# Kernel optimization log

Hardware: AMD Instinct MI355X
Metric: run time of the kernel (lower is better)

## Reference

```python
import jax, jax.numpy as jnp
import numpy as np

B, T, D = 1, 2048, 4096
N, K, H = 32, 8, 128
SLOTS = 32768
THETA = 500000.0
NEG_INF = -1e30


def apply_rope(x, positions, theta=THETA):
    # x: [B, heads, T, H]; positions: [T] int32. Llama half-split rotary.
    h = x.shape[-1]
    inv_freq = 1.0 / (theta ** (jnp.arange(0, h, 2, dtype=jnp.float32) / h))  # [H/2]
    ang = positions.astype(jnp.float32)[:, None] * inv_freq[None, :]          # [T, H/2]
    cos, sin = jnp.cos(ang), jnp.sin(ang)
    x1, x2 = x[..., : h // 2], x[..., h // 2 :]
    return jnp.concatenate([x1 * cos - x2 * sin, x2 * cos + x1 * sin], axis=-1).astype(x.dtype)


def setup_inputs() -> dict:
    key = jax.random.key(0)
    ks = jax.random.split(key, 5)
    x = jax.random.normal(ks[0], (B, T, D), jnp.float32)
    wq = jax.random.normal(ks[1], (N, D, H), jnp.float32) * (D ** -0.5)
    wk = jax.random.normal(ks[2], (K, D, H), jnp.float32) * (D ** -0.5)
    wv = jax.random.normal(ks[3], (K, D, H), jnp.float32) * (D ** -0.5)
    wo = jax.random.normal(ks[4], (N, H, D), jnp.float32) * ((N * H) ** -0.5)
    k_cache = jnp.zeros((SLOTS, K, H), jnp.float32)
    v_cache = jnp.zeros((SLOTS, K, H), jnp.float32)
    positions = jnp.arange(T, dtype=jnp.int32)
    write_indices = jnp.arange(T, dtype=jnp.int32)  # paged-cache slot per token, in [0, SLOTS)
    return dict(x=x, wq=wq, wk=wk, wv=wv, wo=wo, k_cache=k_cache, v_cache=v_cache,
                positions=positions, write_indices=write_indices)


def reference(x, wq, wk, wv, wo, k_cache, v_cache, positions, write_indices):
    # QKV projections (per-head einsum, as in the module)
    q = jnp.einsum('btd,ndh->bnth', x, wq)            # [B,N,T,H]
    k = jnp.einsum('btd,kdh->bkth', x, wk)            # [B,K,T,H]
    v = jnp.einsum('btd,kdh->bkth', x, wv)            # [B,K,T,H]
    # RoPE on q and k, then q scaling by head_dim**-0.5 (applied to q as in source)
    q = apply_rope(q, positions) * (H ** -0.5)
    k = apply_rope(k, positions)
    # KV-cache scatter write (B=1): cache layout [slot, kv_head, head_dim]
    k_cache = k_cache.at[write_indices].set(jnp.transpose(k[0], (1, 0, 2)))
    v_cache = v_cache.at[write_indices].set(jnp.transpose(v[0], (1, 0, 2)))
    # Prefill causal GQA attention over the current sequence
    g = N // K
    qg = q.reshape(B, K, g, T, H)
    scores = jnp.einsum('bkgth,bksh->bkgts', qg, k)   # [B,K,G,T,T]
    mask = positions[:, None] >= positions[None, :]   # causal
    scores = jnp.where(mask, scores, NEG_INF)
    p = jax.nn.softmax(scores, axis=-1)
    attn = jnp.einsum('bkgts,bksh->bkgth', p, v).reshape(B, N, T, H)
    o = jnp.einsum('bnth,nhd->btd', attn, wo)         # [B,T,D]
    return k_cache, v_cache, o
```

## Files before the change

### kernel.cpp

```cpp
#include <hip/hip_runtime.h>
#include <stdint.h>

#define T_SEQ   2048
#define D_MODEL 4096
#define NQ      32
#define NKV     8
#define HD      128
#define NSLOTS  32768
#define L2THETA_64 0.29580575976911624f
#define QSCALE_LOG2E 0.12751743126f

typedef __bf16 bf16;
typedef bf16  bf16x8 __attribute__((ext_vector_type(8)));
typedef float f32x4  __attribute__((ext_vector_type(4)));

#define AS1 __attribute__((address_space(1)))
#define AS3 __attribute__((address_space(3)))

__device__ __forceinline__ void async_ld16(const bf16* g, bf16* l) {
  __builtin_amdgcn_global_load_lds((AS1 void*)(uintptr_t)g, (AS3 void*)l, 16, 0, 0);
}

__global__ __launch_bounds__(256) void convert_bf16(const float* __restrict__ src,
                                                    bf16* __restrict__ dst, int n8) {
  int i = blockIdx.x * blockDim.x + threadIdx.x;
  if (i >= n8) return;
  const float4* s = (const float4*)src + (size_t)i * 2;
  float4 a = s[0], b = s[1];
  bf16x8 o;
  o[0]=(bf16)a.x; o[1]=(bf16)a.y; o[2]=(bf16)a.z; o[3]=(bf16)a.w;
  o[4]=(bf16)b.x; o[5]=(bf16)b.y; o[6]=(bf16)b.z; o[7]=(bf16)b.w;
  *((bf16x8*)dst + i) = o;
}

__global__ __launch_bounds__(256) void transpose_w(const float* __restrict__ src,
                                                   bf16* __restrict__ dst,
                                                   int rows, int cols) {
  __shared__ float tile[32][33];
  const int z = blockIdx.z;
  src += (size_t)z * rows * cols;
  dst += (size_t)z * rows * cols;
  const int c0 = blockIdx.x * 32;
  const int r0 = blockIdx.y * 32;
  const int tx = threadIdx.x;
  const int ty = threadIdx.y;
#pragma unroll
  for (int j = 0; j < 32; j += 8)
    tile[ty + j][tx] = src[(size_t)(r0 + ty + j) * cols + c0 + tx];
  __syncthreads();
#pragma unroll
  for (int j = 0; j < 32; j += 8)
    dst[(size_t)(c0 + ty + j) * rows + r0 + tx] = (bf16)tile[tx][ty + j];
}

__global__ __launch_bounds__(256) void transpose_v(const bf16* __restrict__ src,
                                                   bf16* __restrict__ dst) {
  __shared__ bf16 tile[32][33];
  const int z  = blockIdx.z;
  const int h0 = blockIdx.x * 32;
  const int t0 = blockIdx.y * 32;
  const int tx = threadIdx.x;
  const int ty = threadIdx.y;
  const bf16* s = src + (size_t)z * T_SEQ * HD;
  bf16* d       = dst + (size_t)z * T_SEQ * HD;
#pragma unroll
  for (int j = 0; j < 32; j += 8)
    tile[ty + j][tx] = s[(size_t)(t0 + ty + j) * HD + h0 + tx];
  __syncthreads();
#pragma unroll
  for (int j = 0; j < 32; j += 8)
    d[(size_t)(h0 + ty + j) * T_SEQ + t0 + tx] = tile[tx][ty + j];
}

__global__ __launch_bounds__(256) void gemm_bt(
    const bf16* __restrict__ A, const bf16* __restrict__ Bt, int Kd, int mode,
    bf16* __restrict__ qb, bf16* __restrict__ kb, bf16* __restrict__ vb,
    float* __restrict__ kc_out, float* __restrict__ vc_out,
    const int* __restrict__ positions, const int* __restrict__ wind,
    float* __restrict__ o_out) {
  __shared__ bf16 As[128 * 32];
  __shared__ bf16 Bs[128 * 32];
  const int tid  = threadIdx.x;
  const int wid  = tid >> 6;
  const int lane = tid & 63;
  const int quad = lane >> 4;
  const int l15  = lane & 15;
  const int m0 = blockIdx.x * 128;
  const int n0 = blockIdx.y * 128;

  const int srow = tid >> 2;
  const int scol = (tid & 3) * 8;
  const bf16* Ag0 = A  + (size_t)(m0 + srow) * Kd + scol;
  const bf16* Ag1 = Ag0 + (size_t)64 * Kd;
  const bf16* Bg0 = Bt + (size_t)(n0 + srow) * Kd + scol;
  const bf16* Bg1 = Bg0 + (size_t)64 * Kd;
  bf16* Al0 = As + tid * 8;
  bf16* Al1 = As + (tid + 256) * 8;
  bf16* Bl0 = Bs + tid * 8;
  bf16* Bl1 = Bs + (tid + 256) * 8;

  const f32x4 fz = {0.f, 0.f, 0.f, 0.f};
  f32x4 acc[2][8];
#pragma unroll
  for (int mi = 0; mi < 2; ++mi)
#pragma unroll
    for (int ni = 0; ni < 8; ++ni) acc[mi][ni] = fz;

  const int mrow = wid * 32;
  for (int k0 = 0; k0 < Kd; k0 += 32) {
    async_ld16(Ag0 + k0, Al0);
    async_ld16(Ag1 + k0, Al1);
    async_ld16(Bg0 + k0, Bl0);
    async_ld16(Bg1 + k0, Bl1);
    __syncthreads();
    bf16x8 af[2], bfr[8];
#pragma unroll
    for (int mi = 0; mi < 2; ++mi)
      af[mi] = *(const bf16x8*)(As + (mrow + mi * 16 + l15) * 32 + quad * 8);
#pragma unroll
    for (int ni = 0; ni < 8; ++ni)
      bfr[ni] = *(const bf16x8*)(Bs + (ni * 16 + l15) * 32 + quad * 8);
#pragma unroll
    for (int mi = 0; mi < 2; ++mi)
#pragma unroll
      for (int ni = 0; ni < 8; ++ni)
        acc[mi][ni] = __builtin_amdgcn_mfma_f32_16x16x32_bf16(af[mi], bfr[ni], acc[mi][ni], 0, 0, 0);
    __syncthreads();
  }

  if (mode == 1) {
#pragma unroll
    for (int mi = 0; mi < 2; ++mi)
#pragma unroll
      for (int ni = 0; ni < 8; ++ni)
#pragma unroll
        for (int r = 0; r < 4; ++r) {
          int trow = m0 + mrow + mi * 16 + quad * 4 + r;
          o_out[(size_t)trow * D_MODEL + n0 + ni * 16 + l15] = acc[mi][ni][r];
        }
  } else {
    const int head = blockIdx.y;
#pragma unroll
    for (int mi = 0; mi < 2; ++mi) {
#pragma unroll
      for (int r = 0; r < 4; ++r) {
        const int trow = m0 + mrow + mi * 16 + quad * 4 + r;
        const float pos = (float)positions[trow];
        const int slot = (head >= 32) ? wind[trow] : 0;
#pragma unroll
        for (int ni = 0; ni < 4; ++ni) {
          const int h1 = ni * 16 + l15;
          float a1 = acc[mi][ni][r];
          float a2 = acc[mi][ni + 4][r];
          float o1, o2;
          if (head < 40) {
            float ang = pos * exp2f((float)h1 * -L2THETA_64);
            float sn, cs;
            sincosf(ang, &sn, &cs);
            o1 = a1 * cs - a2 * sn;
            o2 = a2 * cs + a1 * sn;
          } else { o1 = a1; o2 = a2; }
          if (head < 32) {
            o1 *= QSCALE_LOG2E; o2 *= QSCALE_LOG2E;
            bf16* qp = qb + ((size_t)head * T_SEQ + trow) * HD + h1;
            qp[0]  = (bf16)o1;
            qp[64] = (bf16)o2;
          } else if (head < 40) {
            const int kvh = head - 32;
            bf16* kp = kb + ((size_t)kvh * T_SEQ + trow) * HD + h1;
            kp[0]  = (bf16)o1;
            kp[64] = (bf16)o2;
            float* cp = kc_out + ((size_t)slot * NKV + kvh) * HD + h1;
            cp[0]  = o1;
            cp[64] = o2;
          } else {
            const int kvh = head - 40;
            bf16* vp = vb + ((size_t)kvh * T_SEQ + trow) * HD + h1;
            vp[0]  = (bf16)o1;
            vp[64] = (bf16)o2;
            float* cp = vc_out + ((size_t)slot * NKV + kvh) * HD + h1;
            cp[0]  = o1;
            cp[64] = o2;
          }
        }
      }
    }
  }
}

__global__ __launch_bounds__(256, 2) void attn_fused(
    const bf16* __restrict__ qb, const bf16* __restrict__ kb,
    const bf16* __restrict__ vt, bf16* __restrict__ attnb) {
  __shared__ bf16 Ks [64 * 128];
  __shared__ bf16 Vts[128 * 64];
  __shared__ bf16 Ps [4 * 32 * 72];
  const int tid  = threadIdx.x;
  const int wid  = tid >> 6;
  const int lane = tid & 63;
  const int quad = lane >> 4;
  const int l15  = lane & 15;
  const int head = blockIdx.y;
  const int kv   = head >> 2;
  const int bt   = blockIdx.x;
  const int t0b  = bt * 128;
  const int t0w  = t0b + wid * 32;

  bf16x8 qf[2][4];
#pragma unroll
  for (int mi = 0; mi < 2; ++mi) {
    const bf16* qp = qb + ((size_t)head * T_SEQ + t0w + mi * 16 + l15) * HD + quad * 8;
#pragma unroll
    for (int ck = 0; ck < 4; ++ck) qf[mi][ck] = *(const bf16x8*)(qp + ck * 32);
  }

  const f32x4 fz = {0.f, 0.f, 0.f, 0.f};
  f32x4 oacc[2][8];
#pragma unroll
  for (int mi = 0; mi < 2; ++mi)
#pragma unroll
    for (int ch = 0; ch < 8; ++ch) oacc[mi][ch] = fz;
  float l_acc[8];
#pragma unroll
  for (int i = 0; i < 8; ++i) l_acc[i] = 0.f;

  const bf16* kbase = kb + (size_t)kv * T_SEQ * HD;
  const bf16* vbase = vt + (size_t)kv * HD * T_SEQ;
  bf16* Pw = Ps + wid * (32 * 72);

  const int nkt = 2 * bt + 2;
  for (int kt = 0; kt < nkt; ++kt) {
    const int tk0 = kt * 64;
#pragma unroll
    for (int i = 0; i < 4; ++i) {
      const int g = i * 256 + tid;
      const int k = g >> 4, c = g & 15;
      uint4 val = *(const uint4*)(kbase + (size_t)(tk0 + k) * HD + c * 8);
      *(uint4*)(Ks + k * 128 + ((c ^ (k & 15)) * 8)) = val;
    }
#pragma unroll
    for (int i = 0; i < 4; ++i) {
      const int g = i * 256 + tid;
      const int h = g >> 3, c = g & 7;
      uint4 val = *(const uint4*)(vbase + (size_t)h * T_SEQ + tk0 + c * 8);
      *(uint4*)(Vts + h * 64 + ((c ^ (h & 7)) * 8)) = val;
    }
    __syncthreads();

    f32x4 s[2][4];
#pragma unroll
    for (int mi = 0; mi < 2; ++mi)
#pragma unroll
      for (int n = 0; n < 4; ++n) s[mi][n] = fz;
#pragma unroll
    for (int n = 0; n < 4; ++n) {
      const int krow = n * 16 + l15;
#pragma unroll
      for (int ck = 0; ck < 4; ++ck) {
        const int cc = (ck * 4 + quad) ^ (krow & 15);
        bf16x8 kf = *(const bf16x8*)(Ks + krow * 128 + cc * 8);
#pragma unroll
        for (int mi = 0; mi < 2; ++mi)
          s[mi][n] = __builtin_amdgcn_mfma_f32_16x16x32_bf16(qf[mi][ck], kf, s[mi][n], 0, 0, 0);
      }
    }

    const bool domask = (tk0 + 63) > t0w;
#pragma unroll
    for (int mi = 0; mi < 2; ++mi)
#pragma unroll
      for (int r = 0; r < 4; ++r) {
        const int row = t0w + mi * 16 + quad * 4 + r;
#pragma unroll
        for (int n = 0; n < 4; ++n) {
          float p = __builtin_amdgcn_exp2f(s[mi][n][r]);
          if (domask && (tk0 + n * 16 + l15 > row)) p = 0.f;
          l_acc[mi * 4 + r] += p;
          Pw[(mi * 16 + quad * 4 + r) * 72 + n * 16 + l15] = (bf16)p;
        }
      }
    asm volatile("s_waitcnt lgkmcnt(0)" ::: "memory");

#pragma unroll
    for (int kk = 0; kk < 2; ++kk) {
      bf16x8 pf[2];
#pragma unroll
      for (int mi = 0; mi < 2; ++mi)
        pf[mi] = *(const bf16x8*)(Pw + (mi * 16 + l15) * 72 + kk * 32 + quad * 8);
#pragma unroll
      for (int ch = 0; ch < 8; ++ch) {
        const int h = ch * 16 + l15;
        const int cc = (kk * 4 + quad) ^ (h & 7);
        bf16x8 vf = *(const bf16x8*)(Vts + h * 64 + cc * 8);
#pragma unroll
        for (int mi = 0; mi < 2; ++mi)
          oacc[mi][ch] = __builtin_amdgcn_mfma_f32_16x16x32_bf16(pf[mi], vf, oacc[mi][ch], 0, 0, 0);
      }
    }
    __syncthreads();
  }

#pragma unroll
  for (int i = 0; i < 8; ++i) {
    float v = l_acc[i];
#pragma unroll
    for (int off = 1; off < 16; off <<= 1) v += __shfl_xor(v, off);
    l_acc[i] = 1.0f / v;
  }
#pragma unroll
  for (int mi = 0; mi < 2; ++mi)
#pragma unroll
    for (int r = 0; r < 4; ++r) {
      const int trow = t0w + mi * 16 + quad * 4 + r;
      const float inv = l_acc[mi * 4 + r];
#pragma unroll
      for (int ch = 0; ch < 8; ++ch)
        attnb[(size_t)trow * D_MODEL + head * HD + ch * 16 + l15] =
            (bf16)(oacc[mi][ch][r] * inv);
    }
}

extern "C" void kernel_launch(void* const* d_in, const int* in_sizes, int n_in,
                              void* d_out, int out_size, void* d_ws, size_t ws_size,
                              hipStream_t stream) {
  (void)in_sizes; (void)n_in; (void)out_size; (void)ws_size;
  const float* x     = (const float*)d_in[0];
  const float* wq    = (const float*)d_in[1];
  const float* wk    = (const float*)d_in[2];
  const float* wv    = (const float*)d_in[3];
  const float* wo    = (const float*)d_in[4];
  const float* kc_in = (const float*)d_in[5];
  const float* vc_in = (const float*)d_in[6];
  const int* positions = (const int*)d_in[7];
  const int* wind      = (const int*)d_in[8];

  float* out    = (float*)d_out;
  float* kc_out = out;
  float* vc_out = out + (size_t)NSLOTS * NKV * HD;
  float* o_out  = out + (size_t)2 * NSLOTS * NKV * HD;

  char* ws = (char*)d_ws;
  bf16* xb     = (bf16*)(ws);
  bf16* wqkv_t = (bf16*)(ws + (16ull  << 20));
  bf16* wo_t   = (bf16*)(ws + (64ull  << 20));
  bf16* qb     = (bf16*)(ws + (96ull  << 20));
  bf16* kb     = (bf16*)(ws + (112ull << 20));
  bf16* vb     = (bf16*)(ws + (116ull << 20));
  bf16* attnb  = xb;
  bf16* vt     = wqkv_t;

  hipMemcpyAsync(kc_out, kc_in, (size_t)NSLOTS * NKV * HD * 4, hipMemcpyDeviceToDevice, stream);
  hipMemcpyAsync(vc_out, vc_in, (size_t)NSLOTS * NKV * HD * 4, hipMemcpyDeviceToDevice, stream);

  convert_bf16<<<dim3((T_SEQ * D_MODEL / 8 + 255) / 256), dim3(256), 0, stream>>>(
      x, xb, T_SEQ * D_MODEL / 8);
  transpose_w<<<dim3(HD / 32, D_MODEL / 32, NQ),  dim3(32, 8), 0, stream>>>(wq, wqkv_t, D_MODEL, HD);
  transpose_w<<<dim3(HD / 32, D_MODEL / 32, NKV), dim3(32, 8), 0, stream>>>(
      wk, wqkv_t + (size_t)32 * HD * D_MODEL, D_MODEL, HD);
  transpose_w<<<dim3(HD / 32, D_MODEL / 32, NKV), dim3(32, 8), 0, stream>>>(
      wv, wqkv_t + (size_t)40 * HD * D_MODEL, D_MODEL, HD);
  transpose_w<<<dim3(D_MODEL / 32, (NQ * HD) / 32, 1), dim3(32, 8), 0, stream>>>(
      wo, wo_t, NQ * HD, D_MODEL);

  gemm_bt<<<dim3(T_SEQ / 128, 48), dim3(256), 0, stream>>>(
      xb, wqkv_t, D_MODEL, 0, qb, kb, vb, kc_out, vc_out, positions, wind, nullptr);
  transpose_v<<<dim3(HD / 32, T_SEQ / 32, NKV), dim3(32, 8), 0, stream>>>(vb, vt);
  attn_fused<<<dim3(T_SEQ / 128, NQ), dim3(256), 0, stream>>>(qb, kb, vt, attnb);
  gemm_bt<<<dim3(T_SEQ / 128, D_MODEL / 128), dim3(256), 0, stream>>>(
      attnb, wo_t, D_MODEL, 1, nullptr, nullptr, nullptr, nullptr, nullptr,
      nullptr, nullptr, o_out);
}
```

Measured before the change: 948.0 us.

## Fold KV-cache copy into output GEMM, skipping slots overwritten by scatter

Drops the two full-cache device-to-device memcpys. A bitmap of written slots is built from write_indices, and extra blocks appended to the output-projection GEMM grid copy only the unwritten cache slots using nontemporal loads and stores, overlapping this traffic with GEMM compute. The attention kernel also reverses the query-tile order for heads 16 and up to balance causal work across the schedule. This depends on the QKV GEMM having already written the new slots, and the copy now competes with the GEMM for bandwidth.

```diff
diff --git a/kernel.cpp b/kernel.cpp
--- a/kernel.cpp
+++ b/kernel.cpp
@@ -72,15 +72,43 @@
     d[(size_t)(h0 + ty + j) * T_SEQ + t0 + tx] = tile[tx][ty + j];
 }
 
+__global__ __launch_bounds__(256) void mark_slots(const int* __restrict__ wind,
+                                                  uint32_t* __restrict__ bm) {
+  const int tid = threadIdx.x;
+  for (int i = tid; i < NSLOTS / 32; i += 256) bm[i] = 0u;
+  __syncthreads();
+  for (int i = tid; i < T_SEQ; i += 256) {
+    const int s = wind[i];
+    atomicOr(&bm[s >> 5], 1u << (s & 31));
+  }
+}
+
 __global__ __launch_bounds__(256) void gemm_bt(
     const bf16* __restrict__ A, const bf16* __restrict__ Bt, int Kd, int mode,
     bf16* __restrict__ qb, bf16* __restrict__ kb, bf16* __restrict__ vb,
     float* __restrict__ kc_out, float* __restrict__ vc_out,
     const int* __restrict__ positions, const int* __restrict__ wind,
-    float* __restrict__ o_out) {
+    float* __restrict__ o_out,
+    const float* __restrict__ kc_src, const float* __restrict__ vc_src,
+    const uint32_t* __restrict__ slotmap) {
+  const int tid  = threadIdx.x;
+
+  if (mode == 1 && blockIdx.y >= (D_MODEL / 128)) {
+    const int cb   = (blockIdx.y - D_MODEL / 128) * gridDim.x + blockIdx.x;
+    const int nblk = 16 * gridDim.x;
+    for (int s = cb; s < NSLOTS; s += nblk) {
+      if (slotmap[s >> 5] & (1u << (s & 31))) continue;
+      const size_t base = (size_t)s * (NKV * HD);
+      f32x4 kv = __builtin_nontemporal_load((const f32x4*)(kc_src + base) + tid);
+      f32x4 vv = __builtin_nontemporal_load((const f32x4*)(vc_src + base) + tid);
+      __builtin_nontemporal_store(kv, (f32x4*)(kc_out + base) + tid);
+      __builtin_nontemporal_store(vv, (f32x4*)(vc_out + base) + tid);
+    }
+    return;
+  }
+
   __shared__ bf16 As[128 * 32];
   __shared__ bf16 Bs[128 * 32];
-  const int tid  = threadIdx.x;
   const int wid  = tid >> 6;
   const int lane = tid & 63;
   const int quad = lane >> 4;
@@ -201,7 +229,8 @@
   const int l15  = lane & 15;
   const int head = blockIdx.y;
   const int kv   = head >> 2;
-  const int bt   = blockIdx.x;
+  int bt = blockIdx.x;
+  if (head & 16) bt = (T_SEQ / 128 - 1) - bt;
   const int t0b  = bt * 128;
   const int t0w  = t0b + wid * 32;
 
@@ -347,9 +376,7 @@
   bf16* vb     = (bf16*)(ws + (116ull << 20));
   bf16* attnb  = xb;
   bf16* vt     = wqkv_t;
-
-  hipMemcpyAsync(kc_out, kc_in, (size_t)NSLOTS * NKV * HD * 4, hipMemcpyDeviceToDevice, stream);
-  hipMemcpyAsync(vc_out, vc_in, (size_t)NSLOTS * NKV * HD * 4, hipMemcpyDeviceToDevice, stream);
+  uint32_t* slotmap = (uint32_t*)(ws + (24ull << 20));
 
   convert_bf16<<<dim3((T_SEQ * D_MODEL / 8 + 255) / 256), dim3(256), 0, stream>>>(
       x, xb, T_SEQ * D_MODEL / 8);
@@ -362,10 +389,12 @@
       wo, wo_t, NQ * HD, D_MODEL);
 
   gemm_bt<<<dim3(T_SEQ / 128, 48), dim3(256), 0, stream>>>(
-      xb, wqkv_t, D_MODEL, 0, qb, kb, vb, kc_out, vc_out, positions, wind, nullptr);
+      xb, wqkv_t, D_MODEL, 0, qb, kb, vb, kc_out, vc_out, positions, wind, nullptr,
+      nullptr, nullptr, nullptr);
+  mark_slots<<<dim3(1), dim3(256), 0, stream>>>(wind, slotmap);
   transpose_v<<<dim3(HD / 32, T_SEQ / 32, NKV), dim3(32, 8), 0, stream>>>(vb, vt);
   attn_fused<<<dim3(T_SEQ / 128, NQ), dim3(256), 0, stream>>>(qb, kb, vt, attnb);
-  gemm_bt<<<dim3(T_SEQ / 128, D_MODEL / 128), dim3(256), 0, stream>>>(
-      attnb, wo_t, D_MODEL, 1, nullptr, nullptr, nullptr, nullptr, nullptr,
-      nullptr, nullptr, o_out);
-}
+  gemm_bt<<<dim3(T_SEQ / 128, D_MODEL / 128 + 16), dim3(256), 0, stream>>>(
+      attnb, wo_t, D_MODEL, 1, nullptr, nullptr, nullptr, kc_out, vc_out,
+      nullptr, nullptr, o_out, kc_in, vc_in, slotmap);
+}
```

After: 954.6 us. No clear change (+0.7%).
